# Optimization experiments

Hardware: AMD Instinct MI355X
Metric: run time of the kernel (lower is better)

Reference implementation:

```python
import jax, jax.numpy as jnp
import numpy as np

EMBED_DIM = 300
HIDDEN_DIM = 500
NUM_LAYERS = 2
NUM_CLASSES = 20
VOCAB = 100000
SEQ_LEN = 2048


def setup_inputs() -> dict:
    key = jax.random.key(0)
    ks = jax.random.split(key, 12)
    s = 1.0 / np.sqrt(HIDDEN_DIM)
    inp = {
        "sequence": jax.random.randint(ks[0], (SEQ_LEN,), 0, VOCAB),
        "emb": jax.random.normal(ks[1], (VOCAB, EMBED_DIM), jnp.float32),
        # layer 0: input dim 300
        "W_ih0": jax.random.normal(ks[2], (4 * HIDDEN_DIM, EMBED_DIM), jnp.float32) * s,
        "W_hh0": jax.random.normal(ks[3], (4 * HIDDEN_DIM, HIDDEN_DIM), jnp.float32) * s,
        "b_ih0": jax.random.normal(ks[4], (4 * HIDDEN_DIM,), jnp.float32) * s,
        "b_hh0": jax.random.normal(ks[5], (4 * HIDDEN_DIM,), jnp.float32) * s,
        # layer 1: input dim 500
        "W_ih1": jax.random.normal(ks[6], (4 * HIDDEN_DIM, HIDDEN_DIM), jnp.float32) * s,
        "W_hh1": jax.random.normal(ks[7], (4 * HIDDEN_DIM, HIDDEN_DIM), jnp.float32) * s,
        "b_ih1": jax.random.normal(ks[8], (4 * HIDDEN_DIM,), jnp.float32) * s,
        "b_hh1": jax.random.normal(ks[9], (4 * HIDDEN_DIM,), jnp.float32) * s,
        "fc_W": jax.random.normal(ks[10], (NUM_CLASSES, HIDDEN_DIM), jnp.float32) * s,
        "fc_b": jax.random.normal(ks[11], (NUM_CLASSES,), jnp.float32) * s,
    }
    return inp


def _lstm_layer(x_seq, W_ih, W_hh, b_ih, b_hh):
    """Scan a single LSTM layer over the full sequence. x_seq: [T, D_in]."""
    H = W_hh.shape[1]
    # precompute input projections for all timesteps: [T, 4H]
    x_proj = x_seq @ W_ih.T + b_ih + b_hh

    def step(carry, xp):
        h, c = carry
        gates = xp + h @ W_hh.T  # [4H], PyTorch gate order i, f, g, o
        i, f, g, o = jnp.split(gates, 4)
        i = jax.nn.sigmoid(i)
        f = jax.nn.sigmoid(f)
        g = jnp.tanh(g)
        o = jax.nn.sigmoid(o)
        c = f * c + i * g
        h = o * jnp.tanh(c)
        return (h, c), h

    init = (jnp.zeros((H,), x_seq.dtype), jnp.zeros((H,), x_seq.dtype))
    _, hs = jax.lax.scan(step, init, x_proj)
    return hs  # [T, H]


def reference(sequence, emb, W_ih0, W_hh0, b_ih0, b_hh0, W_ih1, W_hh1, b_ih1, b_hh1, fc_W, fc_b):
    x = emb[sequence]                                   # [T, 300]
    h0 = _lstm_layer(x, W_ih0, W_hh0, b_ih0, b_hh0)     # [T, 500]
    h1 = _lstm_layer(h0, W_ih1, W_hh1, b_ih1, b_hh1)    # [T, 500]
    out = h1[-1] @ fc_W.T + fc_b                        # last timestep -> [num_classes]
    return out.reshape(1, -1)
```

## Files before the change

### kernel.cpp

```cpp
#include <hip/hip_runtime.h>

#define T_STEPS 2048
#define H       500
#define E       300
#define HP      512
#define XPT     2048
#define NCLS    20
#define NB0     125
#define NB1     125
#define BIAS2   2.0f

typedef float v4f __attribute__((ext_vector_type(4)));

__device__ __forceinline__ float sigm_(float x){ return 1.0f/(1.0f+__expf(-x)); }
__device__ __forceinline__ float tanh_(float x){ return 2.0f/(1.0f+__expf(-2.0f*x)) - 1.0f; }

__device__ __forceinline__ v4f v4z() { v4f r; r.x=0.f; r.y=0.f; r.z=0.f; r.w=0.f; return r; }
__device__ __forceinline__ v4f v4sub(v4f v, float s){ v4f r; r.x=v.x-s; r.y=v.y-s; r.z=v.z-s; r.w=v.w-s; return r; }
__device__ __forceinline__ bool nz4(v4f v){ return v.x!=0.f && v.y!=0.f && v.z!=0.f && v.w!=0.f; }
__device__ __forceinline__ float dot4(v4f w, v4f x){ return w.x*x.x + w.y*x.y + w.z*x.z + w.w*x.w; }

__device__ __forceinline__ void poll2(const float* p0, const float* p1, v4f& a, v4f& b) {
    asm volatile("global_load_dwordx4 %0, %2, off sc0 sc1\n\t"
                 "global_load_dwordx4 %1, %3, off sc0 sc1\n\t"
                 "s_waitcnt vmcnt(0)"
                 : "=&v"(a), "=&v"(b)
                 : "v"(p0), "v"(p1));
}
__device__ __forceinline__ void store1_cc(float* p, float v) {
    asm volatile("global_store_dword %0, %1, off sc0 sc1" :: "v"(p), "v"(v));
}

__global__ __launch_bounds__(256) void lstm_init(float* hs) {
    int i = blockIdx.x*256 + threadIdx.x;
    const int NH4 = (T_STEPS+1)*HP/4;
    v4f b2; b2.x=BIAS2; b2.y=BIAS2; b2.z=BIAS2; b2.w=BIAS2;
    bool seed = (i < H/4) || (i >= NH4 && i < NH4 + H/4);
    ((v4f*)hs)[i] = seed ? b2 : v4z();
}

__global__ __launch_bounds__(256) void xproj_kernel(
    const int* __restrict__ seq, const float* __restrict__ emb,
    const float* __restrict__ Wih0, const float* __restrict__ bih0,
    const float* __restrict__ bhh0, float* __restrict__ xp)
{
    __shared__ float xe[16][308];
    const int tid = threadIdx.x;
    const int t0 = blockIdx.x * 16;
    for (int i = tid; i < 16*76; i += 256) {
        int tt = i / 76, c4 = (i - tt*76) * 4;
        v4f val = v4z();
        if (c4 < E) val = *(const v4f*)&emb[(size_t)seq[t0+tt]*E + c4];
        *(v4f*)&xe[tt][c4] = val;
    }
    __syncthreads();
    const int rg = tid >> 4, tl = tid & 15;
    for (int k = 0; k < 125; ++k) {
        int row = k*16 + rg;
        const float* wr = Wih0 + (size_t)row*E;
        float acc = bih0[row] + bhh0[row];
        #pragma unroll 5
        for (int c = 0; c < 75; ++c)
            acc += dot4(*(const v4f*)(wr + 4*c), *(const v4f*)&xe[tl][4*c]);
        xp[(size_t)row*XPT + t0 + tl] = acc;
    }
}

__device__ __forceinline__ float reduce16(float* acc, int lane) {
    float v8[8];
    {
        const bool b = lane & 1;
        #pragma unroll
        for (int i = 0; i < 8; ++i) {
            float keep = b ? acc[8+i] : acc[i];
            float send = b ? acc[i]   : acc[8+i];
            v8[i] = keep + __shfl_xor(send, 1, 64);
        }
    }
    float v4a[4];
    {
        const bool b = lane & 2;
        #pragma unroll
        for (int i = 0; i < 4; ++i) {
            float keep = b ? v8[4+i] : v8[i];
            float send = b ? v8[i]   : v8[4+i];
            v4a[i] = keep + __shfl_xor(send, 2, 64);
        }
    }
    float v2a[2];
    {
        const bool b = lane & 4;
        #pragma unroll
        for (int i = 0; i < 2; ++i) {
            float keep = b ? v4a[2+i] : v4a[i];
            float send = b ? v4a[i]   : v4a[2+i];
            v2a[i] = keep + __shfl_xor(send, 4, 64);
        }
    }
    float v1;
    {
        const bool b = lane & 8;
        float keep = b ? v2a[1] : v2a[0];
        float send = b ? v2a[0] : v2a[1];
        v1 = keep + __shfl_xor(send, 8, 64);
    }
    v1 += __shfl_xor(v1, 16, 64);
    v1 += __shfl_xor(v1, 32, 64);
    return v1;
}

__device__ __forceinline__ float gates_combine(float x, int b2, int b3, float& cs) {
    const bool isG = (b2 == 1 && b3 == 0);
    float a = 1.f/(1.f + __expf(isG ? -2.f*x : -x));
    float act = isG ? 2.f*a - 1.f : a;
    float t1 = __shfl_xor(act, 4, 64);
    float t2 = __shfl_xor(act, 8, 64);
    float t3 = __shfl_xor(act, 12, 64);
    float gi = b2 ? (b3 ? t3 : t1) : (b3 ? t2 : act);
    float gf = b2 ? (b3 ? t1 : t3) : (b3 ? act : t2);
    float gg = b2 ? (b3 ? t2 : act) : (b3 ? t3 : t1);
    float go = b2 ? (b3 ? act : t2) : (b3 ? t1 : t3);
    cs = gf*cs + gi*gg;
    return go * tanh_(cs);
}

__launch_bounds__(128, 1)
__global__ void lstm_main(
    const float* __restrict__ Whh0,
    const float* __restrict__ Wih1, const float* __restrict__ Whh1,
    const float* __restrict__ bih1, const float* __restrict__ bhh1,
    const float* __restrict__ fcW, const float* __restrict__ fcb,
    float* __restrict__ out,
    const float* __restrict__ xp, float* h0s, float* h1s)
{
    __shared__ float part[2][64];
    const int blk  = blockIdx.x;
    const int wid  = threadIdx.x >> 6;
    const int lane = threadIdx.x & 63;
    const int c0 = 8*lane;
    const bool need0 = (c0 + 4 <= H);
    const bool need1 = (c0 + 8 <= H);
    const int b0 = lane&1, b1=(lane>>1)&1, b2=(lane>>2)&1, b3=(lane>>3)&1;
    const int unit = 2*b0 + b1;
    const int gate = 2*b2 + b3;

    if (blk < NB0) {
        if (wid == 1) return;
        const int u0 = 4*blk;
        v4f w[16][2];
        #pragma unroll
        for (int r = 0; r < 16; ++r) {
            const int R_ = (r&3)*H + u0 + (r>>2);
            const float* wh = Whh0 + (size_t)R_*H;
            w[r][0] = need0 ? *(const v4f*)(wh + c0)     : v4z();
            w[r][1] = need1 ? *(const v4f*)(wh + c0 + 4) : v4z();
        }
        const float* xpp = xp + (size_t)(gate*H + u0 + unit)*XPT;
        float cs = 0.f;

        for (int t = 1; t <= T_STEPS; ++t) {
            float xpv = xpp[t-1];
            const float* hp = h0s + (size_t)(t-1)*HP;
            v4f A = v4z(), B = v4z();
            bool ok = !(need0 || need1);
            while (!__all(ok)) {
                if (!ok) {
                    poll2(hp + c0, hp + c0 + 4, A, B);
                    ok = (!need0 || nz4(A)) && (!need1 || nz4(B));
                }
            }
            v4f i0 = v4sub(A, BIAS2), i1 = v4sub(B, BIAS2);
            float acc[16];
            #pragma unroll
            for (int r = 0; r < 16; ++r)
                acc[r] = dot4(w[r][0], i0) + dot4(w[r][1], i1);
            float v = reduce16(acc, lane);
            float hval = gates_combine(v + xpv, b2, b3, cs);
            if ((lane & 60) == 0)
                store1_cc(h0s + (size_t)t*HP + u0 + unit, hval + BIAS2);
        }
    } else {
        const int g  = blk - NB0;
        const int u0 = 4*g;
        if (wid == 0) {
            v4f w[16][2];
            float bsum;
            {
                const int R_ = gate*H + u0 + unit;
                bsum = bih1[R_] + bhh1[R_];
            }
            #pragma unroll
            for (int r = 0; r < 16; ++r) {
                const int R_ = (r&3)*H + u0 + (r>>2);
                const float* wi = Wih1 + (size_t)R_*H;
                w[r][0] = need0 ? *(const v4f*)(wi + c0)     : v4z();
                w[r][1] = need1 ? *(const v4f*)(wi + c0 + 4) : v4z();
            }
            float cs = 0.f;
            for (int t = 1; t <= T_STEPS; ++t) {
                const float* hp = h0s + (size_t)t*HP;
                v4f A = v4z(), B = v4z();
                bool ok = !(need0 || need1);
                while (!__all(ok)) {
                    if (!ok) {
                        poll2(hp + c0, hp + c0 + 4, A, B);
                        ok = (!need0 || nz4(A)) && (!need1 || nz4(B));
                    }
                }
                v4f i0 = v4sub(A, BIAS2), i1 = v4sub(B, BIAS2);
                float acc[16];
                #pragma unroll
                for (int r = 0; r < 16; ++r)
                    acc[r] = dot4(w[r][0], i0) + dot4(w[r][1], i1);
                float v = reduce16(acc, lane);
                __syncthreads();
                v += part[t&1][lane];
                float hval = gates_combine(v + bsum, b2, b3, cs);
                if ((lane & 60) == 0)
                    store1_cc(h1s + (size_t)t*HP + u0 + unit, hval + BIAS2);
            }
            if (g == 0) {
                const float* hT = h1s + (size_t)T_STEPS*HP;
                v4f A = v4z(), B = v4z();
                bool ok = !(need0 || need1);
                while (!__all(ok)) {
                    if (!ok) {
                        poll2(hT + c0, hT + c0 + 4, A, B);
                        ok = (!need0 || nz4(A)) && (!need1 || nz4(B));
                    }
                }
                v4f h0v = need0 ? v4sub(A, BIAS2) : v4z();
                v4f h1v = need1 ? v4sub(B, BIAS2) : v4z();
                #pragma unroll 4
                for (int r = 0; r < NCLS; ++r) {
                    const float* wr = fcW + (size_t)r*H;
                    v4f wa = need0 ? *(const v4f*)(wr + c0)     : v4z();
                    v4f wb = need1 ? *(const v4f*)(wr + c0 + 4) : v4z();
                    float a = dot4(wa, h0v) + dot4(wb, h1v);
                    #pragma unroll
                    for (int m = 32; m >= 1; m >>= 1) a += __shfl_xor(a, m, 64);
                    if (lane == 0) out[r] = a + fcb[r];
                }
            }
        } else {
            v4f w[16][2];
            #pragma unroll
            for (int r = 0; r < 16; ++r) {
                const int R_ = (r&3)*H + u0 + (r>>2);
                const float* wh = Whh1 + (size_t)R_*H;
                w[r][0] = need0 ? *(const v4f*)(wh + c0)     : v4z();
                w[r][1] = need1 ? *(const v4f*)(wh + c0 + 4) : v4z();
            }
            for (int t = 1; t <= T_STEPS; ++t) {
                const float* hp = h1s + (size_t)(t-1)*HP;
                v4f A = v4z(), B = v4z();
                bool ok = !(need0 || need1);
                while (!__all(ok)) {
                    if (!ok) {
                        poll2(hp + c0, hp + c0 + 4, A, B);
                        ok = (!need0 || nz4(A)) && (!need1 || nz4(B));
                    }
                }
                v4f i0 = v4sub(A, BIAS2), i1 = v4sub(B, BIAS2);
                float acc[16];
                #pragma unroll
                for (int r = 0; r < 16; ++r)
                    acc[r] = dot4(w[r][0], i0) + dot4(w[r][1], i1);
                part[t&1][lane] = reduce16(acc, lane);
                __syncthreads();
            }
        }
    }
}

extern "C" void kernel_launch(void* const* d_in, const int* in_sizes, int n_in,
                              void* d_out, int out_size, void* d_ws, size_t ws_size,
                              hipStream_t stream)
{
    const int*   seq  = (const int*)d_in[0];
    const float* emb  = (const float*)d_in[1];
    const float* Whh0 = (const float*)d_in[3];
    const float* bih0 = (const float*)d_in[4];
    const float* bhh0 = (const float*)d_in[5];
    const float* Wih0 = (const float*)d_in[2];
    const float* Wih1 = (const float*)d_in[6];
    const float* Whh1 = (const float*)d_in[7];
    const float* bih1 = (const float*)d_in[8];
    const float* bhh1 = (const float*)d_in[9];
    const float* fcW  = (const float*)d_in[10];
    const float* fcb  = (const float*)d_in[11];
    float* out = (float*)d_out;

    float* h0s = (float*)d_ws;
    float* h1s = h0s + (size_t)(T_STEPS+1)*HP;
    float* xpj = h1s + (size_t)(T_STEPS+1)*HP;

    hipLaunchKernelGGL(lstm_init, dim3(2049), dim3(256), 0, stream, h0s);
    hipLaunchKernelGGL(xproj_kernel, dim3(T_STEPS/16), dim3(256), 0, stream,
                       seq, emb, Wih0, bih0, bhh0, xpj);
    hipLaunchKernelGGL(lstm_main, dim3(NB0 + NB1), dim3(128), 0, stream,
                       Whh0, Wih1, Whh1, bih1, bhh1, fcW, fcb, out, xpj, h0s, h1s);
}
```

Before: 5.896 ms.

## Fuse input projection into persistent LSTM kernel with replicated ring-buffer handoff

Drops the separate xproj kernel and computes the layer-0 input projection inside the recurrent loop from embedding rows. Hidden-state exchange moves from full-sequence arrays to small ring buffers with sign-alternating validity flags, replicated four times so pollers spread across copies. Each block now uses four waves that split the dot-product columns and combine partial sums through shared memory. Layer-0 producers also wait on a lagged layer-1 slot as backpressure so the rings are not overwritten early. The cost is extra per-step Wih0 loads, a block barrier every step, and four stores per hidden value.

Result: faster. 5.150 ms (-12.7%).

```diff
diff --git a/kernel.cpp b/kernel.cpp
--- a/kernel.cpp
+++ b/kernel.cpp
@@ -4,112 +4,101 @@
 #define H       500
 #define E       300
 #define HP      512
-#define XPT     2048
 #define NCLS    20
 #define NB0     125
 #define NB1     125
-#define BIAS2   2.0f
-
+#define NREP    4
+#define K0      8
+#define K1      4
+#define THR_LAG 4
+
+typedef float v2f __attribute__((ext_vector_type(2)));
 typedef float v4f __attribute__((ext_vector_type(4)));
 
-__device__ __forceinline__ float sigm_(float x){ return 1.0f/(1.0f+__expf(-x)); }
 __device__ __forceinline__ float tanh_(float x){ return 2.0f/(1.0f+__expf(-2.0f*x)) - 1.0f; }
-
-__device__ __forceinline__ v4f v4z() { v4f r; r.x=0.f; r.y=0.f; r.z=0.f; r.w=0.f; return r; }
-__device__ __forceinline__ v4f v4sub(v4f v, float s){ v4f r; r.x=v.x-s; r.y=v.y-s; r.z=v.z-s; r.w=v.w-s; return r; }
-__device__ __forceinline__ bool nz4(v4f v){ return v.x!=0.f && v.y!=0.f && v.z!=0.f && v.w!=0.f; }
+__device__ __forceinline__ v2f v2z(){ v2f r; r.x=0.f; r.y=0.f; return r; }
+__device__ __forceinline__ v4f v4z(){ v4f r; r.x=0.f; r.y=0.f; r.z=0.f; r.w=0.f; return r; }
 __device__ __forceinline__ float dot4(v4f w, v4f x){ return w.x*x.x + w.y*x.y + w.z*x.z + w.w*x.w; }
 
-__device__ __forceinline__ void poll2(const float* p0, const float* p1, v4f& a, v4f& b) {
+__device__ __forceinline__ float s0f(int t){ return ((t>>3)&1) ? -1.f : 1.f; }
+__device__ __forceinline__ float s1f(int t){ return ((t>>2)&1) ? -1.f : 1.f; }
+
+__device__ __forceinline__ bool valid2(v2f v, float s){
+    return (s > 0.f) ? (v.x > 0.5f && v.y > 0.5f) : (v.x < -0.5f && v.y < -0.5f);
+}
+__device__ __forceinline__ bool valid4(v4f v, float s){
+    return (s > 0.f) ? (v.x > 0.5f && v.y > 0.5f && v.z > 0.5f && v.w > 0.5f)
+                     : (v.x < -0.5f && v.y < -0.5f && v.z < -0.5f && v.w < -0.5f);
+}
+
+__device__ __forceinline__ void pollx2_2(const float* p0, const float* p1, v2f& a, v2f& b){
+    asm volatile("global_load_dwordx2 %0, %2, off sc0 sc1\n\t"
+                 "global_load_dwordx2 %1, %3, off sc0 sc1\n\t"
+                 "s_waitcnt vmcnt(0)"
+                 : "=&v"(a), "=&v"(b) : "v"(p0), "v"(p1));
+}
+__device__ __forceinline__ v4f pollx4(const float* p){
+    v4f a;
+    asm volatile("global_load_dwordx4 %0, %1, off sc0 sc1\n\ts_waitcnt vmcnt(0)"
+                 : "=&v"(a) : "v"(p));
+    return a;
+}
+__device__ __forceinline__ void pollx4_2(const float* p0, const float* p1, v4f& a, v4f& b){
     asm volatile("global_load_dwordx4 %0, %2, off sc0 sc1\n\t"
                  "global_load_dwordx4 %1, %3, off sc0 sc1\n\t"
                  "s_waitcnt vmcnt(0)"
-                 : "=&v"(a), "=&v"(b)
-                 : "v"(p0), "v"(p1));
-}
-__device__ __forceinline__ void store1_cc(float* p, float v) {
+                 : "=&v"(a), "=&v"(b) : "v"(p0), "v"(p1));
+}
+__device__ __forceinline__ void store1_cc(float* p, float v){
     asm volatile("global_store_dword %0, %1, off sc0 sc1" :: "v"(p), "v"(v));
 }
 
-__global__ __launch_bounds__(256) void lstm_init(float* hs) {
+__global__ __launch_bounds__(256) void lstm_init(float* h0rep, float* h1rep){
     int i = blockIdx.x*256 + threadIdx.x;
-    const int NH4 = (T_STEPS+1)*HP/4;
-    v4f b2; b2.x=BIAS2; b2.y=BIAS2; b2.z=BIAS2; b2.w=BIAS2;
-    bool seed = (i < H/4) || (i >= NH4 && i < NH4 + H/4);
-    ((v4f*)hs)[i] = seed ? b2 : v4z();
-}
-
-__global__ __launch_bounds__(256) void xproj_kernel(
-    const int* __restrict__ seq, const float* __restrict__ emb,
-    const float* __restrict__ Wih0, const float* __restrict__ bih0,
-    const float* __restrict__ bhh0, float* __restrict__ xp)
-{
-    __shared__ float xe[16][308];
-    const int tid = threadIdx.x;
-    const int t0 = blockIdx.x * 16;
-    for (int i = tid; i < 16*76; i += 256) {
-        int tt = i / 76, c4 = (i - tt*76) * 4;
-        v4f val = v4z();
-        if (c4 < E) val = *(const v4f*)&emb[(size_t)seq[t0+tt]*E + c4];
-        *(v4f*)&xe[tt][c4] = val;
+    if (i < NREP*K0*HP) {
+        int rem = i % (K0*HP), slot = rem / HP, col = rem % HP;
+        h0rep[i] = (slot == 0 && col < H) ? 2.0f : 0.f;
     }
-    __syncthreads();
-    const int rg = tid >> 4, tl = tid & 15;
-    for (int k = 0; k < 125; ++k) {
-        int row = k*16 + rg;
-        const float* wr = Wih0 + (size_t)row*E;
-        float acc = bih0[row] + bhh0[row];
-        #pragma unroll 5
-        for (int c = 0; c < 75; ++c)
-            acc += dot4(*(const v4f*)(wr + 4*c), *(const v4f*)&xe[tl][4*c]);
-        xp[(size_t)row*XPT + t0 + tl] = acc;
+    int i1 = i - NREP*K0*HP;
+    if (i1 >= 0 && i1 < NREP*K1*HP) {
+        int rem = i1 % (K1*HP), slot = rem / HP, col = rem % HP;
+        h1rep[i1] = (slot == 0 && col < H) ? 2.0f : 0.f;
     }
 }
 
-__device__ __forceinline__ float reduce16(float* acc, int lane) {
+__device__ __forceinline__ float reduce16(float* acc, int lane){
     float v8[8];
-    {
-        const bool b = lane & 1;
-        #pragma unroll
-        for (int i = 0; i < 8; ++i) {
-            float keep = b ? acc[8+i] : acc[i];
-            float send = b ? acc[i]   : acc[8+i];
-            v8[i] = keep + __shfl_xor(send, 1, 64);
-        }
-    }
+    { const bool b = lane & 1;
+      #pragma unroll
+      for (int i = 0; i < 8; ++i){
+        float keep = b ? acc[8+i] : acc[i];
+        float send = b ? acc[i]   : acc[8+i];
+        v8[i] = keep + __shfl_xor(send, 1, 64); } }
     float v4a[4];
-    {
-        const bool b = lane & 2;
-        #pragma unroll
-        for (int i = 0; i < 4; ++i) {
-            float keep = b ? v8[4+i] : v8[i];
-            float send = b ? v8[i]   : v8[4+i];
-            v4a[i] = keep + __shfl_xor(send, 2, 64);
-        }
-    }
+    { const bool b = lane & 2;
+      #pragma unroll
+      for (int i = 0; i < 4; ++i){
+        float keep = b ? v8[4+i] : v8[i];
+        float send = b ? v8[i]   : v8[4+i];
+        v4a[i] = keep + __shfl_xor(send, 2, 64); } }
     float v2a[2];
-    {
-        const bool b = lane & 4;
-        #pragma unroll
-        for (int i = 0; i < 2; ++i) {
-            float keep = b ? v4a[2+i] : v4a[i];
-            float send = b ? v4a[i]   : v4a[2+i];
-            v2a[i] = keep + __shfl_xor(send, 4, 64);
-        }
-    }
+    { const bool b = lane & 4;
+      #pragma unroll
+      for (int i = 0; i < 2; ++i){
+        float keep = b ? v4a[2+i] : v4a[i];
+        float send = b ? v4a[i]   : v4a[2+i];
+        v2a[i] = keep + __shfl_xor(send, 4, 64); } }
     float v1;
-    {
-        const bool b = lane & 8;
-        float keep = b ? v2a[1] : v2a[0];
-        float send = b ? v2a[0] : v2a[1];
-        v1 = keep + __shfl_xor(send, 8, 64);
-    }
+    { const bool b = lane & 8;
+      float keep = b ? v2a[1] : v2a[0];
+      float send = b ? v2a[0] : v2a[1];
+      v1 = keep + __shfl_xor(send, 8, 64); }
     v1 += __shfl_xor(v1, 16, 64);
     v1 += __shfl_xor(v1, 32, 64);
     return v1;
 }
 
-__device__ __forceinline__ float gates_combine(float x, int b2, int b3, float& cs) {
+__device__ __forceinline__ float gates16(float x, int b2, int b3, float& cs){
     const bool isG = (b2 == 1 && b3 == 0);
     float a = 1.f/(1.f + __expf(isG ? -2.f*x : -x));
     float act = isG ? 2.f*a - 1.f : a;
@@ -124,150 +113,183 @@
     return go * tanh_(cs);
 }
 
-__launch_bounds__(128, 1)
+__launch_bounds__(256, 1)
 __global__ void lstm_main(
-    const float* __restrict__ Whh0,
+    const int* __restrict__ seq, const float* __restrict__ emb,
+    const float* __restrict__ Wih0, const float* __restrict__ Whh0,
+    const float* __restrict__ bih0, const float* __restrict__ bhh0,
     const float* __restrict__ Wih1, const float* __restrict__ Whh1,
     const float* __restrict__ bih1, const float* __restrict__ bhh1,
     const float* __restrict__ fcW, const float* __restrict__ fcb,
     float* __restrict__ out,
-    const float* __restrict__ xp, float* h0s, float* h1s)
+    float* h0rep, float* h1rep)
 {
-    __shared__ float part[2][64];
-    const int blk  = blockIdx.x;
-    const int wid  = threadIdx.x >> 6;
-    const int lane = threadIdx.x & 63;
-    const int c0 = 8*lane;
-    const bool need0 = (c0 + 4 <= H);
-    const bool need1 = (c0 + 8 <= H);
-    const int b0 = lane&1, b1=(lane>>1)&1, b2=(lane>>2)&1, b3=(lane>>3)&1;
+    __shared__ float part[2][3][16];
+
+    const int blk = blockIdx.x;
+    const int wid = (int)(threadIdx.x >> 6);
+    const int j   = (int)(threadIdx.x & 63);
+    const int b0 = j&1, b1=(j>>1)&1, b2=(j>>2)&1, b3=(j>>3)&1;
     const int unit = 2*b0 + b1;
     const int gate = 2*b2 + b3;
+    const int rep  = (blk + wid) & (NREP-1);
 
     if (blk < NB0) {
-        if (wid == 1) return;
         const int u0 = 4*blk;
-        v4f w[16][2];
+        const int cw = 128*wid + 2*j;
+        const bool hAct = (cw < H);
+        const bool xAct = (cw < E);
+
+        v2f w2[16];
         #pragma unroll
         for (int r = 0; r < 16; ++r) {
             const int R_ = (r&3)*H + u0 + (r>>2);
-            const float* wh = Whh0 + (size_t)R_*H;
-            w[r][0] = need0 ? *(const v4f*)(wh + c0)     : v4z();
-            w[r][1] = need1 ? *(const v4f*)(wh + c0 + 4) : v4z();
-        }
-        const float* xpp = xp + (size_t)(gate*H + u0 + unit)*XPT;
+            w2[r] = hAct ? *(const v2f*)(Whh0 + (size_t)R_*H + cw) : v2z();
+        }
+        float bs = 0.f;
+        if (wid == 0) { const int R_my = gate*H + u0 + unit; bs = bih0[R_my] + bhh0[R_my]; }
+
         float cs = 0.f;
+        v2f xcur = xAct ? *(const v2f*)(emb + (size_t)seq[0]*E + cw) : v2z();
+
+        float* h0base = h0rep + (size_t)rep*K0*HP;
+        float* h1base = h1rep + (size_t)rep*K1*HP;
 
         for (int t = 1; t <= T_STEPS; ++t) {
-            float xpv = xpp[t-1];
-            const float* hp = h0s + (size_t)(t-1)*HP;
-            v4f A = v4z(), B = v4z();
-            bool ok = !(need0 || need1);
-            while (!__all(ok)) {
-                if (!ok) {
-                    poll2(hp + c0, hp + c0 + 4, A, B);
-                    ok = (!need0 || nz4(A)) && (!need1 || nz4(B));
-                }
-            }
-            v4f i0 = v4sub(A, BIAS2), i1 = v4sub(B, BIAS2);
+            v2f xn = v2z();
+            if (xAct && t < T_STEPS) xn = *(const v2f*)(emb + (size_t)seq[t]*E + cw);
+
             float acc[16];
             #pragma unroll
+            for (int r = 0; r < 16; ++r) {
+                const int R_ = (r&3)*H + u0 + (r>>2);
+                v2f wi = xAct ? *(const v2f*)(Wih0 + (size_t)R_*E + cw) : v2z();
+                acc[r] = wi.x*xcur.x + wi.y*xcur.y;
+            }
+
+            const float sM = s0f(t-1);
+            const int tau = (t > THR_LAG) ? t - THR_LAG : 0;
+            const float sT = s1f(tau);
+            const float* pm = h0base + (size_t)((t-1)&(K0-1))*HP + cw;
+            const float* pt = h1base + (size_t)(tau&(K1-1))*HP + cw;
+            v2f Mv = v2z(); bool gm = !hAct, gt = !hAct;
+            while (!__all(gm && gt)) {
+                if (!(gm && gt)) {
+                    v2f m, th;
+                    pollx2_2(pm, pt, m, th);
+                    if (!gm && valid2(m, sM)) { Mv = m; gm = true; }
+                    if (!gt && valid2(th, sT)) gt = true;
+                }
+            }
+
+            v2f hd; hd.x = __builtin_fmaf(Mv.x, sM, -2.f); hd.y = __builtin_fmaf(Mv.y, sM, -2.f);
+            #pragma unroll
             for (int r = 0; r < 16; ++r)
-                acc[r] = dot4(w[r][0], i0) + dot4(w[r][1], i1);
-            float v = reduce16(acc, lane);
-            float hval = gates_combine(v + xpv, b2, b3, cs);
-            if ((lane & 60) == 0)
-                store1_cc(h0s + (size_t)t*HP + u0 + unit, hval + BIAS2);
+                acc[r] += w2[r].x*hd.x + w2[r].y*hd.y;
+
+            float red = reduce16(acc, j);
+
+            if (wid != 0) { if (j < 16) part[t&1][wid-1][j] = red; }
+            __syncthreads();
+            if (wid == 0) {
+                float val = red + part[t&1][0][j&15] + part[t&1][1][j&15] + part[t&1][2][j&15] + bs;
+                float hval = gates16(val, b2, b3, cs);
+                if ((j & 60) == 0) {
+                    const float sv = s0f(t);
+                    const float outv = (hval + 2.f) * sv;
+                    const size_t off = (size_t)(t&(K0-1))*HP + u0 + unit;
+                    #pragma unroll
+                    for (int rr = 0; rr < NREP; ++rr)
+                        store1_cc(h0rep + (size_t)rr*K0*HP + off, outv);
+                }
+            }
+            xcur = xn;
         }
     } else {
         const int g  = blk - NB0;
         const int u0 = 4*g;
-        if (wid == 0) {
-            v4f w[16][2];
-            float bsum;
-            {
-                const int R_ = gate*H + u0 + unit;
-                bsum = bih1[R_] + bhh1[R_];
-            }
+        const int c4 = ((wid&1) ? 256 : 0) + 4*j;
+        const bool act = (c4 < H);
+        const bool isIH = (wid < 2);
+        const float* Wsel = isIH ? Wih1 : Whh1;
+
+        v4f wv[16];
+        #pragma unroll
+        for (int r = 0; r < 16; ++r) {
+            const int R_ = (r&3)*H + u0 + (r>>2);
+            wv[r] = act ? *(const v4f*)(Wsel + (size_t)R_*H + c4) : v4z();
+        }
+        float bs = 0.f;
+        if (wid == 0) { const int R_my = gate*H + u0 + unit; bs = bih1[R_my] + bhh1[R_my]; }
+
+        float cs = 0.f;
+        float* h0base = h0rep + (size_t)rep*K0*HP;
+        float* h1base = h1rep + (size_t)rep*K1*HP;
+
+        for (int t = 1; t <= T_STEPS; ++t) {
+            const float s = isIH ? s0f(t) : s1f(t-1);
+            const float* pm = isIH ? (h0base + (size_t)(t&(K0-1))*HP + c4)
+                                   : (h1base + (size_t)((t-1)&(K1-1))*HP + c4);
+            v4f Av = v4z(); bool gm = !act;
+            while (!__all(gm)) {
+                if (!gm) {
+                    v4f a = pollx4(pm);
+                    if (valid4(a, s)) { Av = a; gm = true; }
+                }
+            }
+            v4f hd;
+            hd.x = __builtin_fmaf(Av.x, s, -2.f); hd.y = __builtin_fmaf(Av.y, s, -2.f);
+            hd.z = __builtin_fmaf(Av.z, s, -2.f); hd.w = __builtin_fmaf(Av.w, s, -2.f);
+
+            float acc[16];
             #pragma unroll
-            for (int r = 0; r < 16; ++r) {
-                const int R_ = (r&3)*H + u0 + (r>>2);
-                const float* wi = Wih1 + (size_t)R_*H;
-                w[r][0] = need0 ? *(const v4f*)(wi + c0)     : v4z();
-                w[r][1] = need1 ? *(const v4f*)(wi + c0 + 4) : v4z();
-            }
-            float cs = 0.f;
-            for (int t = 1; t <= T_STEPS; ++t) {
-                const float* hp = h0s + (size_t)t*HP;
-                v4f A = v4z(), B = v4z();
-                bool ok = !(need0 || need1);
-                while (!__all(ok)) {
-                    if (!ok) {
-                        poll2(hp + c0, hp + c0 + 4, A, B);
-                        ok = (!need0 || nz4(A)) && (!need1 || nz4(B));
-                    }
-                }
-                v4f i0 = v4sub(A, BIAS2), i1 = v4sub(B, BIAS2);
-                float acc[16];
+            for (int r = 0; r < 16; ++r) acc[r] = dot4(wv[r], hd);
+
+            float red = reduce16(acc, j);
+
+            if (wid != 0) { if (j < 16) part[t&1][wid-1][j] = red; }
+            __syncthreads();
+            if (wid == 0) {
+                float val = red + part[t&1][0][j&15] + part[t&1][1][j&15] + part[t&1][2][j&15] + bs;
+                float hval = gates16(val, b2, b3, cs);
+                if ((j & 60) == 0) {
+                    const float sv = s1f(t);
+                    const float outv = (hval + 2.f) * sv;
+                    const size_t off = (size_t)(t&(K1-1))*HP + u0 + unit;
+                    #pragma unroll
+                    for (int rr = 0; rr < NREP; ++rr)
+                        store1_cc(h1rep + (size_t)rr*K1*HP + off, outv);
+                }
+            }
+        }
+
+        if (g == 0 && wid == 0) {
+            const int cA = 4*j, cB = 256 + 4*j;
+            const bool hasB = (cB + 4 <= H);
+            const float* hT = h1rep + (size_t)(T_STEPS&(K1-1))*HP;
+            const float sfin = s1f(T_STEPS);
+            v4f Alat = v4z(), Blat = v4z(); bool ga = false, gb = !hasB;
+            while (!__all(ga && gb)) {
+                if (!(ga && gb)) {
+                    v4f a, b;
+                    pollx4_2(hT + cA, hT + cB, a, b);
+                    if (!ga && valid4(a, sfin)) { Alat = a; ga = true; }
+                    if (!gb && valid4(b, sfin)) { Blat = b; gb = true; }
+                }
+            }
+            v4f v0, v1;
+            v0.x=Alat.x-2.f; v0.y=Alat.y-2.f; v0.z=Alat.z-2.f; v0.w=Alat.w-2.f;
+            v1.x=Blat.x-2.f; v1.y=Blat.y-2.f; v1.z=Blat.z-2.f; v1.w=Blat.w-2.f;
+            if (!hasB) v1 = v4z();
+            #pragma unroll 4
+            for (int r = 0; r < NCLS; ++r) {
+                const float* wr = fcW + (size_t)r*H;
+                v4f fa = *(const v4f*)(wr + cA);
+                v4f fb = hasB ? *(const v4f*)(wr + cB) : v4z();
+                float a = dot4(fa, v0) + dot4(fb, v1);
                 #pragma unroll
-                for (int r = 0; r < 16; ++r)
-                    acc[r] = dot4(w[r][0], i0) + dot4(w[r][1], i1);
-                float v = reduce16(acc, lane);
-                __syncthreads();
-                v += part[t&1][lane];
-                float hval = gates_combine(v + bsum, b2, b3, cs);
-                if ((lane & 60) == 0)
-                    store1_cc(h1s + (size_t)t*HP + u0 + unit, hval + BIAS2);
-            }
-            if (g == 0) {
-                const float* hT = h1s + (size_t)T_STEPS*HP;
-                v4f A = v4z(), B = v4z();
-                bool ok = !(need0 || need1);
-                while (!__all(ok)) {
-                    if (!ok) {
-                        poll2(hT + c0, hT + c0 + 4, A, B);
-                        ok = (!need0 || nz4(A)) && (!need1 || nz4(B));
-                    }
-                }
-                v4f h0v = need0 ? v4sub(A, BIAS2) : v4z();
-                v4f h1v = need1 ? v4sub(B, BIAS2) : v4z();
-                #pragma unroll 4
-                for (int r = 0; r < NCLS; ++r) {
-                    const float* wr = fcW + (size_t)r*H;
-                    v4f wa = need0 ? *(const v4f*)(wr + c0)     : v4z();
-                    v4f wb = need1 ? *(const v4f*)(wr + c0 + 4) : v4z();
-                    float a = dot4(wa, h0v) + dot4(wb, h1v);
-                    #pragma unroll
-                    for (int m = 32; m >= 1; m >>= 1) a += __shfl_xor(a, m, 64);
-                    if (lane == 0) out[r] = a + fcb[r];
-                }
-            }
-        } else {
-            v4f w[16][2];
-            #pragma unroll
-            for (int r = 0; r < 16; ++r) {
-                const int R_ = (r&3)*H + u0 + (r>>2);
-                const float* wh = Whh1 + (size_t)R_*H;
-                w[r][0] = need0 ? *(const v4f*)(wh + c0)     : v4z();
-                w[r][1] = need1 ? *(const v4f*)(wh + c0 + 4) : v4z();
-            }
-            for (int t = 1; t <= T_STEPS; ++t) {
-                const float* hp = h1s + (size_t)(t-1)*HP;
-                v4f A = v4z(), B = v4z();
-                bool ok = !(need0 || need1);
-                while (!__all(ok)) {
-                    if (!ok) {
-                        poll2(hp + c0, hp + c0 + 4, A, B);
-                        ok = (!need0 || nz4(A)) && (!need1 || nz4(B));
-                    }
-                }
-                v4f i0 = v4sub(A, BIAS2), i1 = v4sub(B, BIAS2);
-                float acc[16];
-                #pragma unroll
-                for (int r = 0; r < 16; ++r)
-                    acc[r] = dot4(w[r][0], i0) + dot4(w[r][1], i1);
-                part[t&1][lane] = reduce16(acc, lane);
-                __syncthreads();
+                for (int m = 32; m >= 1; m >>= 1) a += __shfl_xor(a, m, 64);
+                if (j == 0) out[r] = a + fcb[r];
             }
         }
     }
@@ -279,10 +301,10 @@
 {
     const int*   seq  = (const int*)d_in[0];
     const float* emb  = (const float*)d_in[1];
+    const float* Wih0 = (const float*)d_in[2];
     const float* Whh0 = (const float*)d_in[3];
     const float* bih0 = (const float*)d_in[4];
     const float* bhh0 = (const float*)d_in[5];
-    const float* Wih0 = (const float*)d_in[2];
     const float* Wih1 = (const float*)d_in[6];
     const float* Whh1 = (const float*)d_in[7];
     const float* bih1 = (const float*)d_in[8];
@@ -291,13 +313,11 @@
     const float* fcb  = (const float*)d_in[11];
     float* out = (float*)d_out;
 
-    float* h0s = (float*)d_ws;
-    float* h1s = h0s + (size_t)(T_STEPS+1)*HP;
-    float* xpj = h1s + (size_t)(T_STEPS+1)*HP;
-
-    hipLaunchKernelGGL(lstm_init, dim3(2049), dim3(256), 0, stream, h0s);
-    hipLaunchKernelGGL(xproj_kernel, dim3(T_STEPS/16), dim3(256), 0, stream,
-                       seq, emb, Wih0, bih0, bhh0, xpj);
-    hipLaunchKernelGGL(lstm_main, dim3(NB0 + NB1), dim3(128), 0, stream,
-                       Whh0, Wih1, Whh1, bih1, bhh1, fcW, fcb, out, xpj, h0s, h1s);
-}
+    float* h0rep = (float*)d_ws;
+    float* h1rep = h0rep + (size_t)NREP*K0*HP;
+
+    hipLaunchKernelGGL(lstm_init, dim3(96), dim3(256), 0, stream, h0rep, h1rep);
+    hipLaunchKernelGGL(lstm_main, dim3(NB0 + NB1), dim3(256), 0, stream,
+                       seq, emb, Wih0, Whh0, bih0, bhh0, Wih1, Whh1, bih1, bhh1,
+                       fcW, fcb, out, h0rep, h1rep);
+}
```
